# Kernel optimization log

Measured on AMD Instinct MI355X. Metric: run time of the kernel, lower is better.

## Reference

```python
import jax, jax.numpy as jnp
import numpy as np

D_MODEL = 1024
N_HEADS = 16
HEAD_DIM = D_MODEL // N_HEADS


def setup_inputs() -> dict:
    key = jax.random.key(0)
    ks = jax.random.split(key, 5)
    B, S = 4, 2048
    scale = 1.0 / np.sqrt(D_MODEL)
    return {
        "x": jax.random.normal(ks[0], (B, S, D_MODEL), dtype=jnp.float32),
        "W_q": jax.random.normal(ks[1], (D_MODEL, D_MODEL), dtype=jnp.float32) * scale,
        "W_k": jax.random.normal(ks[2], (D_MODEL, D_MODEL), dtype=jnp.float32) * scale,
        "W_v": jax.random.normal(ks[3], (D_MODEL, D_MODEL), dtype=jnp.float32) * scale,
        "W_o": jax.random.normal(ks[4], (D_MODEL, D_MODEL), dtype=jnp.float32) * scale,
    }


def reference(x, W_q, W_k, W_v, W_o):
    B, S, _ = x.shape
    # nn.Linear(d,d,bias=False): y = x @ W.T ; W stored as (out,in)
    def proj(W):
        y = jnp.einsum('bsd,ed->bse', x, W)
        return y.reshape(B, S, N_HEADS, HEAD_DIM).transpose(0, 2, 1, 3)  # (B,H,S,Dh)
    q, k, v = proj(W_q), proj(W_k), proj(W_v)
    scores = jnp.einsum('bhqd,bhkd->bhqk', q, k) / np.sqrt(HEAD_DIM)
    causal = jnp.tril(jnp.ones((S, S), dtype=bool))  # (S,S)
    scores = jnp.where(causal[None, None], scores, -jnp.inf)
    attn = jax.nn.softmax(scores, axis=-1)
    heads = jnp.einsum('bhqk,bhkd->bhqd', attn, v)
    concat = heads.transpose(0, 2, 1, 3).reshape(B, S, D_MODEL)
    return jnp.einsum('bsd,ed->bse', concat, W_o)
```

## Files before the change

### kernel.cpp

```cpp
#include <hip/hip_runtime.h>
#include <hip/hip_bf16.h>

#define D_MODEL 1024
#define N_HEADS 16
#define HEAD_DIM 64
#define BATCH 4
#define SEQ 2048
#define M_ROWS (BATCH * SEQ)

typedef __attribute__((ext_vector_type(8))) __bf16 bf16x8;
typedef __attribute__((ext_vector_type(8))) short short8;
typedef __attribute__((ext_vector_type(4))) float f32x4;

static __device__ __forceinline__ unsigned short f2bf_rne(float f) {
  unsigned int u = __float_as_uint(f);
  u += 0x7FFFu + ((u >> 16) & 1u);
  return (unsigned short)(u >> 16);
}

#if __has_builtin(__builtin_amdgcn_exp2f)
#define EXP2F(x) __builtin_amdgcn_exp2f(x)
#else
#define EXP2F(x) exp2f(x)
#endif

static __device__ __forceinline__ void gl_lds16(const unsigned short* g, unsigned short* l) {
  __builtin_amdgcn_global_load_lds((const __attribute__((address_space(1))) unsigned int*)g,
                                   (__attribute__((address_space(3))) unsigned int*)l, 16, 0, 0);
}

__global__ __launch_bounds__(256) void cvt_all(const float* __restrict__ x,
                                               const float* __restrict__ wq,
                                               const float* __restrict__ wk,
                                               const float* __restrict__ wv,
                                               const float* __restrict__ wo,
                                               unsigned short* __restrict__ xb,
                                               unsigned short* __restrict__ wqb,
                                               unsigned short* __restrict__ wkb,
                                               unsigned short* __restrict__ wvb,
                                               unsigned short* __restrict__ wob) {
  const int bid = blockIdx.x;
  const float* src;
  unsigned short* dst;
  int i;
  if (bid < 8192) {
    src = x; dst = xb; i = bid * 256 + threadIdx.x;
  } else {
    int r = bid - 8192;
    int w = r >> 10;
    i = (r & 1023) * 256 + threadIdx.x;
    switch (w) {
      case 0: src = wq; dst = wqb; break;
      case 1: src = wk; dst = wkb; break;
      case 2: src = wv; dst = wvb; break;
      default: src = wo; dst = wob; break;
    }
  }
  float4 f = reinterpret_cast<const float4*>(src)[i];
  ushort4 o;
  o.x = f2bf_rne(f.x); o.y = f2bf_rne(f.y); o.z = f2bf_rne(f.z); o.w = f2bf_rne(f.w);
  reinterpret_cast<ushort4*>(dst)[i] = o;
}

__global__ __launch_bounds__(256) void qkv_gemm(const unsigned short* __restrict__ A,
                                                const unsigned short* __restrict__ Wq,
                                                const unsigned short* __restrict__ Wk,
                                                const unsigned short* __restrict__ Wv,
                                                unsigned short* __restrict__ Qo,
                                                unsigned short* __restrict__ Ko,
                                                unsigned short* __restrict__ Vt) {
  __shared__ __align__(16) unsigned short smem[16384];
  const int t = threadIdx.x;
  const int widx = blockIdx.x >> 3;
  const int bn = blockIdx.x & 7, bm = blockIdx.y;
  const unsigned short* Bw = (widx == 0) ? Wq : (widx == 1) ? Wk : Wv;
  const float oscale = (widx == 0) ? 0.18033688f : 1.0f;
  const int K = D_MODEL, N = D_MODEL;

  const int wave = t >> 6, lane = t & 63;
  const int wm = (wave >> 1) * 64, wn = (wave & 1) * 64;
  const int lr = lane & 15, quad = lane >> 4;
  const int rxor = (lr >> 1) & 3;

  const int g0 = wave * 128 + lane, g1 = g0 + 64;
  const int r0 = g0 >> 2, c0 = (((g0 & 3) ^ ((r0 >> 1) & 3)) << 3);
  const int r1 = g1 >> 2, c1 = (((g1 & 3) ^ ((r1 >> 1) & 3)) << 3);
  const unsigned short* Arow0 = A + (size_t)(bm * 128 + r0) * K + c0;
  const unsigned short* Arow1 = A + (size_t)(bm * 128 + r1) * K + c1;
  const unsigned short* Brow0 = Bw + (size_t)(bn * 128 + r0) * K + c0;
  const unsigned short* Brow1 = Bw + (size_t)(bn * 128 + r1) * K + c1;

  f32x4 acc[4][4] = {};

  gl_lds16(Arow0, &smem[g0 * 8]);
  gl_lds16(Arow1, &smem[g1 * 8]);
  gl_lds16(Brow0, &smem[4096 + g0 * 8]);
  gl_lds16(Brow1, &smem[4096 + g1 * 8]);
  __syncthreads();

  for (int it = 0; it < 32; it++) {
    const int cur = (it & 1) * 8192;
    if (it + 1 < 32) {
      const int nxt = 8192 - cur;
      const int k1 = (it + 1) * 32;
      gl_lds16(Arow0 + k1, &smem[nxt + g0 * 8]);
      gl_lds16(Arow1 + k1, &smem[nxt + g1 * 8]);
      gl_lds16(Brow0 + k1, &smem[nxt + 4096 + g0 * 8]);
      gl_lds16(Brow1 + k1, &smem[nxt + 4096 + g1 * 8]);
    }
    const unsigned short* As = &smem[cur];
    const unsigned short* Bs = &smem[cur + 4096];

    bf16x8 af[4], bfr[4];
#pragma unroll
    for (int mt = 0; mt < 4; mt++)
      af[mt] = __builtin_bit_cast(
          bf16x8,
          *reinterpret_cast<const short8*>(&As[(wm + mt * 16 + lr) * 32 + (quad ^ rxor) * 8]));
#pragma unroll
    for (int nt = 0; nt < 4; nt++)
      bfr[nt] = __builtin_bit_cast(
          bf16x8,
          *reinterpret_cast<const short8*>(&Bs[(wn + nt * 16 + lr) * 32 + (quad ^ rxor) * 8]));
#pragma unroll
    for (int mt = 0; mt < 4; mt++)
#pragma unroll
      for (int nt = 0; nt < 4; nt++)
        acc[mt][nt] = __builtin_amdgcn_mfma_f32_16x16x32_bf16(af[mt], bfr[nt], acc[mt][nt], 0, 0, 0);
    __syncthreads();
  }

  if (widx < 2) {
    unsigned short* Cp = (widx == 0) ? Qo : Ko;
#pragma unroll
    for (int mt = 0; mt < 4; mt++) {
#pragma unroll
      for (int nt = 0; nt < 4; nt++) {
        int col = bn * 128 + wn + nt * 16 + lr;
#pragma unroll
        for (int r = 0; r < 4; r++) {
          int row = bm * 128 + wm + mt * 16 + quad * 4 + r;
          Cp[(size_t)row * N + col] = f2bf_rne(acc[mt][nt][r] * oscale);
        }
      }
    }
  } else {
    const int b = bm >> 4;
    const int s0 = (bm & 15) * 128;
#pragma unroll
    for (int half = 0; half < 2; half++) {
      __syncthreads();
      if ((wave & 1) == half) {
#pragma unroll
        for (int nt = 0; nt < 4; nt++) {
#pragma unroll
          for (int mt = 0; mt < 4; mt++) {
#pragma unroll
            for (int r = 0; r < 4; r++) {
              int cl = nt * 16 + lr;
              int rl = wm + mt * 16 + quad * 4 + r;
              smem[cl * 136 + rl] = f2bf_rne(acc[mt][nt][r]);
            }
          }
        }
      }
      __syncthreads();
      const int h2 = bn * 2 + half;
      const size_t rowbase = ((size_t)(b * N_HEADS + h2)) * HEAD_DIM;
#pragma unroll
      for (int i = 0; i < 4; i++) {
        int c = i * 256 + t;
        int d = c >> 4, s8 = (c & 15) * 8;
        uint4 v = *reinterpret_cast<const uint4*>(&smem[d * 136 + s8]);
        *reinterpret_cast<uint4*>(Vt + (rowbase + d) * SEQ + s0 + s8) = v;
      }
    }
  }
}

__global__ __launch_bounds__(256) void gemm_bt_f32(const unsigned short* __restrict__ A,
                                                   const unsigned short* __restrict__ Bw,
                                                   float* __restrict__ Cp,
                                                   int M, int N, int K) {
  __shared__ __align__(16) unsigned short smem[16384];
  const int t = threadIdx.x;
  const int bn = blockIdx.x, bm = blockIdx.y;
  const int wave = t >> 6, lane = t & 63;
  const int wm = (wave >> 1) * 64, wn = (wave & 1) * 64;
  const int lr = lane & 15, quad = lane >> 4;
  const int rxor = (lr >> 1) & 3;

  const int g0 = wave * 128 + lane, g1 = g0 + 64;
  const int r0 = g0 >> 2, c0 = (((g0 & 3) ^ ((r0 >> 1) & 3)) << 3);
  const int r1 = g1 >> 2, c1 = (((g1 & 3) ^ ((r1 >> 1) & 3)) << 3);
  const unsigned short* Arow0 = A + (size_t)(bm * 128 + r0) * K + c0;
  const unsigned short* Arow1 = A + (size_t)(bm * 128 + r1) * K + c1;
  const unsigned short* Brow0 = Bw + (size_t)(bn * 128 + r0) * K + c0;
  const unsigned short* Brow1 = Bw + (size_t)(bn * 128 + r1) * K + c1;

  f32x4 acc[4][4] = {};

  gl_lds16(Arow0, &smem[g0 * 8]);
  gl_lds16(Arow1, &smem[g1 * 8]);
  gl_lds16(Brow0, &smem[4096 + g0 * 8]);
  gl_lds16(Brow1, &smem[4096 + g1 * 8]);
  __syncthreads();

  for (int it = 0; it < 32; it++) {
    const int cur = (it & 1) * 8192;
    if (it + 1 < 32) {
      const int nxt = 8192 - cur;
      const int k1 = (it + 1) * 32;
      gl_lds16(Arow0 + k1, &smem[nxt + g0 * 8]);
      gl_lds16(Arow1 + k1, &smem[nxt + g1 * 8]);
      gl_lds16(Brow0 + k1, &smem[nxt + 4096 + g0 * 8]);
      gl_lds16(Brow1 + k1, &smem[nxt + 4096 + g1 * 8]);
    }
    const unsigned short* As = &smem[cur];
    const unsigned short* Bs = &smem[cur + 4096];

    bf16x8 af[4], bfr[4];
#pragma unroll
    for (int mt = 0; mt < 4; mt++)
      af[mt] = __builtin_bit_cast(
          bf16x8,
          *reinterpret_cast<const short8*>(&As[(wm + mt * 16 + lr) * 32 + (quad ^ rxor) * 8]));
#pragma unroll
    for (int nt = 0; nt < 4; nt++)
      bfr[nt] = __builtin_bit_cast(
          bf16x8,
          *reinterpret_cast<const short8*>(&Bs[(wn + nt * 16 + lr) * 32 + (quad ^ rxor) * 8]));
#pragma unroll
    for (int mt = 0; mt < 4; mt++)
#pragma unroll
      for (int nt = 0; nt < 4; nt++)
        acc[mt][nt] = __builtin_amdgcn_mfma_f32_16x16x32_bf16(af[mt], bfr[nt], acc[mt][nt], 0, 0, 0);
    __syncthreads();
  }

#pragma unroll
  for (int mt = 0; mt < 4; mt++) {
#pragma unroll
    for (int nt = 0; nt < 4; nt++) {
      int col = bn * 128 + wn + nt * 16 + lr;
#pragma unroll
      for (int r = 0; r < 4; r++) {
        int row = bm * 128 + wm + mt * 16 + quad * 4 + r;
        Cp[(size_t)row * N + col] = acc[mt][nt][r];
      }
    }
  }
}

__global__ __launch_bounds__(512, 4) void attn_causal(const unsigned short* __restrict__ Q,
                                                      const unsigned short* __restrict__ Km,
                                                      const unsigned short* __restrict__ Vt,
                                                      unsigned short* __restrict__ O) {
  __shared__ __align__(16) unsigned short Kv[2][2][64 * 64];
  __shared__ __align__(16) unsigned short Ps[8][16 * 72];

  const int bid = blockIdx.x;
  const int p = bid & 7;
  const int h = (bid >> 3) & 15;
  const int b = bid >> 7;

  const int t = threadIdx.x;
  const int wave = t >> 6, lane = t & 63;
  const int lr = lane & 15, quad = lane >> 4;
  const int cxor = lr & 7;

  const size_t base = (size_t)b * SEQ * D_MODEL + h * HEAD_DIM;
  const unsigned short* Qb = Q + base;
  const unsigned short* Kb = Km + base;
  const unsigned short* Vb = Vt + (size_t)(b * N_HEADS + h) * HEAD_DIM * SEQ;
  unsigned short* pw = &Ps[wave][0];

  const int srow = t >> 3;
  const int scol = ((t & 7) ^ (srow & 7)) << 3;
  const unsigned short* Kg = Kb + (size_t)srow * D_MODEL + scol;
  const unsigned short* Vg = Vb + (size_t)srow * SEQ + scol;

  for (int ph = 0; ph < 2; ph++) {
    const int qt = ph ? (15 - p) : p;
    const int m0 = qt * 128 + wave * 16;
    const int ntiles = (qt + 1) * 2;

    bf16x8 qf[2];
#pragma unroll
    for (int kk = 0; kk < 2; kk++)
      qf[kk] = __builtin_bit_cast(
          bf16x8,
          *reinterpret_cast<const short8*>(Qb + (size_t)(m0 + lr) * D_MODEL + kk * 32 + quad * 8));

    f32x4 o_acc[4] = {};
    float lsum[4] = {};

    gl_lds16(Kg, &Kv[0][0][t * 8]);
    gl_lds16(Vg, &Kv[0][1][t * 8]);

    for (int kt = 0; kt < ntiles; kt++) {
      const int cur = kt & 1;
      const int kv0 = kt * 64;
      __syncthreads();
      if (kt + 1 < ntiles) {
        gl_lds16(Kg + (size_t)(kv0 + 64) * D_MODEL, &Kv[1 - cur][0][t * 8]);
        gl_lds16(Vg + kv0 + 64, &Kv[1 - cur][1][t * 8]);
      }
      const unsigned short* Ks = &Kv[cur][0][0];
      const unsigned short* Vs = &Kv[cur][1][0];

      f32x4 sAcc[4] = {};
#pragma unroll
      for (int kk = 0; kk < 2; kk++) {
        bf16x8 kf[4];
#pragma unroll
        for (int j = 0; j < 4; j++)
          kf[j] = __builtin_bit_cast(
              bf16x8, *reinterpret_cast<const short8*>(
                          &Ks[(j * 16 + lr) * 64 + ((kk * 4 + quad) ^ cxor) * 8]));
#pragma unroll
        for (int j = 0; j < 4; j++)
          sAcc[j] = __builtin_amdgcn_mfma_f32_16x16x32_bf16(qf[kk], kf[j], sAcc[j], 0, 0, 0);
      }

      asm volatile("s_waitcnt lgkmcnt(0)" ::: "memory");
      const bool needmask = (kv0 + 63 > m0);
#pragma unroll
      for (int r = 0; r < 4; r++) {
        const int qpos = m0 + quad * 4 + r;
        float e[4];
#pragma unroll
        for (int j = 0; j < 4; j++) e[j] = EXP2F(sAcc[j][r]);
        if (needmask) {
#pragma unroll
          for (int j = 0; j < 4; j++)
            if (kv0 + j * 16 + lr > qpos) e[j] = 0.f;
        }
        lsum[r] += (e[0] + e[1]) + (e[2] + e[3]);
        unsigned short* pr = &pw[(quad * 4 + r) * 72];
#pragma unroll
        for (int j = 0; j < 4; j++) pr[j * 16 + lr] = f2bf_rne(e[j]);
      }
      asm volatile("s_waitcnt lgkmcnt(0)" ::: "memory");

#pragma unroll
      for (int kk = 0; kk < 2; kk++) {
        bf16x8 pf = __builtin_bit_cast(
            bf16x8, *reinterpret_cast<const short8*>(&pw[lr * 72 + kk * 32 + quad * 8]));
#pragma unroll
        for (int c = 0; c < 4; c++) {
          bf16x8 vv = __builtin_bit_cast(
              bf16x8, *reinterpret_cast<const short8*>(
                          &Vs[(c * 16 + lr) * 64 + ((kk * 4 + quad) ^ cxor) * 8]));
          o_acc[c] = __builtin_amdgcn_mfma_f32_16x16x32_bf16(pf, vv, o_acc[c], 0, 0, 0);
        }
      }
    }

#pragma unroll
    for (int r = 0; r < 4; r++) {
      float l = lsum[r];
#pragma unroll
      for (int off = 1; off < 16; off <<= 1) l += __shfl_xor(l, off, 64);
      const float inv = 1.f / l;
      const int qpos = m0 + quad * 4 + r;
#pragma unroll
      for (int c = 0; c < 4; c++)
        O[base + (size_t)qpos * D_MODEL + c * 16 + lr] = f2bf_rne(o_acc[c][r] * inv);
    }
  }
}

extern "C" void kernel_launch(void* const* d_in, const int* in_sizes, int n_in,
                              void* d_out, int out_size, void* d_ws, size_t ws_size,
                              hipStream_t stream) {
  const float* x  = (const float*)d_in[0];
  const float* Wq = (const float*)d_in[1];
  const float* Wk = (const float*)d_in[2];
  const float* Wv = (const float*)d_in[3];
  const float* Wo = (const float*)d_in[4];
  float* out = (float*)d_out;

  char* ws = (char*)d_ws;
  const size_t SZ_X = (size_t)M_ROWS * D_MODEL * 2;
  const size_t SZ_W = (size_t)D_MODEL * D_MODEL * 2;
  unsigned short* xb  = (unsigned short*)(ws);
  unsigned short* wqb = (unsigned short*)(ws + SZ_X);
  unsigned short* wkb = (unsigned short*)(ws + SZ_X + 1 * SZ_W);
  unsigned short* wvb = (unsigned short*)(ws + SZ_X + 2 * SZ_W);
  unsigned short* wob = (unsigned short*)(ws + SZ_X + 3 * SZ_W);
  unsigned short* Qb  = (unsigned short*)(ws + 1 * SZ_X + 4 * SZ_W);
  unsigned short* Kb  = (unsigned short*)(ws + 2 * SZ_X + 4 * SZ_W);
  unsigned short* Vt  = (unsigned short*)(ws + 3 * SZ_X + 4 * SZ_W);
  unsigned short* Ob  = xb;

  cvt_all<<<12288, 256, 0, stream>>>(x, Wq, Wk, Wv, Wo, xb, wqb, wkb, wvb, wob);

  qkv_gemm<<<dim3(24, 64), 256, 0, stream>>>(xb, wqb, wkb, wvb, Qb, Kb, Vt);

  attn_causal<<<512, 512, 0, stream>>>(Qb, Kb, Vt, Ob);

  gemm_bt_f32<<<dim3(8, 64), 256, 0, stream>>>(Ob, wob, out, M_ROWS, D_MODEL, D_MODEL);
}
```

Baseline: 259.3 us.

## Rewrite QKV GEMM as 256x256 8-wave pipelined kernel with setprio

Replaces the 128x128, 4-wave QKV projection GEMM with a 256x256-tile, 512-thread kernel. It uses a 64-wide K step, 128 KB of LDS staging and a hand-scheduled prefetch interleaved with the MFMA phases via explicit barriers and vmcnt waits, plus a remapped block order for L2 locality. The aim is more operand reuse per loaded byte and better overlap of global loads with compute. It also raises wave priority around MFMA blocks in the attention kernel. Risks are lower occupancy, high register pressure from 32 accumulators, and subtle synchronization errors in the custom pipeline.

Measured after the change: 245.9 us. -5.2%, faster.

```diff
diff --git a/kernel.cpp b/kernel.cpp
--- a/kernel.cpp
+++ b/kernel.cpp
@@ -28,6 +28,10 @@
   __builtin_amdgcn_global_load_lds((const __attribute__((address_space(1))) unsigned int*)g,
                                    (__attribute__((address_space(3))) unsigned int*)l, 16, 0, 0);
 }
+
+#define BAR() asm volatile("s_barrier" ::: "memory")
+#define WAIT_LGKM0() asm volatile("s_waitcnt lgkmcnt(0)" ::: "memory")
+#define WAIT_VM(N) asm volatile("s_waitcnt vmcnt(" #N ")" ::: "memory")
 
 __global__ __launch_bounds__(256) void cvt_all(const float* __restrict__ x,
                                                const float* __restrict__ wq,
@@ -62,117 +66,157 @@
   reinterpret_cast<ushort4*>(dst)[i] = o;
 }
 
-__global__ __launch_bounds__(256) void qkv_gemm(const unsigned short* __restrict__ A,
-                                                const unsigned short* __restrict__ Wq,
-                                                const unsigned short* __restrict__ Wk,
-                                                const unsigned short* __restrict__ Wv,
-                                                unsigned short* __restrict__ Qo,
-                                                unsigned short* __restrict__ Ko,
-                                                unsigned short* __restrict__ Vt) {
-  __shared__ __align__(16) unsigned short smem[16384];
+__global__ __launch_bounds__(512, 2) void qkv_gemm8(const unsigned short* __restrict__ A,
+                                                    const unsigned short* __restrict__ Wq,
+                                                    const unsigned short* __restrict__ Wk,
+                                                    const unsigned short* __restrict__ Wv,
+                                                    unsigned short* __restrict__ Qo,
+                                                    unsigned short* __restrict__ Ko,
+                                                    unsigned short* __restrict__ Vt) {
+  __shared__ __align__(16) unsigned short smem[65536];
+
+  const int bid = blockIdx.x;
+  const int wgid = (bid & 7) * 48 + (bid >> 3);
+  const int widx = wgid >> 7;
+  const int rem = wgid & 127;
+  const int bm = rem >> 2, bn = rem & 3;
+
+  const unsigned short* Bw = (widx == 0) ? Wq : (widx == 1) ? Wk : Wv;
+
   const int t = threadIdx.x;
-  const int widx = blockIdx.x >> 3;
-  const int bn = blockIdx.x & 7, bm = blockIdx.y;
-  const unsigned short* Bw = (widx == 0) ? Wq : (widx == 1) ? Wk : Wv;
-  const float oscale = (widx == 0) ? 0.18033688f : 1.0f;
-  const int K = D_MODEL, N = D_MODEL;
-
   const int wave = t >> 6, lane = t & 63;
-  const int wm = (wave >> 1) * 64, wn = (wave & 1) * 64;
+  const int wmi = wave >> 2, wni = wave & 3;
   const int lr = lane & 15, quad = lane >> 4;
-  const int rxor = (lr >> 1) & 3;
-
-  const int g0 = wave * 128 + lane, g1 = g0 + 64;
-  const int r0 = g0 >> 2, c0 = (((g0 & 3) ^ ((r0 >> 1) & 3)) << 3);
-  const int r1 = g1 >> 2, c1 = (((g1 & 3) ^ ((r1 >> 1) & 3)) << 3);
-  const unsigned short* Arow0 = A + (size_t)(bm * 128 + r0) * K + c0;
-  const unsigned short* Arow1 = A + (size_t)(bm * 128 + r1) * K + c1;
-  const unsigned short* Brow0 = Bw + (size_t)(bn * 128 + r0) * K + c0;
-  const unsigned short* Brow1 = Bw + (size_t)(bn * 128 + r1) * K + c1;
-
-  f32x4 acc[4][4] = {};
-
-  gl_lds16(Arow0, &smem[g0 * 8]);
-  gl_lds16(Arow1, &smem[g1 * 8]);
-  gl_lds16(Brow0, &smem[4096 + g0 * 8]);
-  gl_lds16(Brow1, &smem[4096 + g1 * 8]);
-  __syncthreads();
-
-  for (int it = 0; it < 32; it++) {
-    const int cur = (it & 1) * 8192;
-    if (it + 1 < 32) {
-      const int nxt = 8192 - cur;
-      const int k1 = (it + 1) * 32;
-      gl_lds16(Arow0 + k1, &smem[nxt + g0 * 8]);
-      gl_lds16(Arow1 + k1, &smem[nxt + g1 * 8]);
-      gl_lds16(Brow0 + k1, &smem[nxt + 4096 + g0 * 8]);
-      gl_lds16(Brow1 + k1, &smem[nxt + 4096 + g1 * 8]);
-    }
-    const unsigned short* As = &smem[cur];
-    const unsigned short* Bs = &smem[cur + 4096];
-
-    bf16x8 af[4], bfr[4];
-#pragma unroll
-    for (int mt = 0; mt < 4; mt++)
-      af[mt] = __builtin_bit_cast(
-          bf16x8,
-          *reinterpret_cast<const short8*>(&As[(wm + mt * 16 + lr) * 32 + (quad ^ rxor) * 8]));
-#pragma unroll
-    for (int nt = 0; nt < 4; nt++)
-      bfr[nt] = __builtin_bit_cast(
-          bf16x8,
-          *reinterpret_cast<const short8*>(&Bs[(wn + nt * 16 + lr) * 32 + (quad ^ rxor) * 8]));
-#pragma unroll
-    for (int mt = 0; mt < 4; mt++)
-#pragma unroll
-      for (int nt = 0; nt < 4; nt++)
-        acc[mt][nt] = __builtin_amdgcn_mfma_f32_16x16x32_bf16(af[mt], bfr[nt], acc[mt][nt], 0, 0, 0);
-    __syncthreads();
+
+  const int r0 = t >> 3, c0 = (t & 7) ^ (r0 & 7);
+  const int s1 = t + 512;
+  const int r1 = s1 >> 3, c1 = (s1 & 7) ^ (r1 & 7);
+  const unsigned short* Asrc0 = A + (size_t)(bm * 256 + r0) * D_MODEL + c0 * 8;
+  const unsigned short* Asrc1 = A + (size_t)(bm * 256 + r1) * D_MODEL + c1 * 8;
+  const unsigned short* Bsrc0 = Bw + (size_t)(bn * 256 + r0) * D_MODEL + c0 * 8;
+  const unsigned short* Bsrc1 = Bw + (size_t)(bn * 256 + r1) * D_MODEL + c1 * 8;
+
+  auto stageA = [&](int kt, int buf, int half) {
+    unsigned short* dst = &smem[(buf * 2 + half) * 8192];
+    const size_t go = (size_t)half * (128 * D_MODEL) + kt * 64;
+    gl_lds16(Asrc0 + go, dst + t * 8);
+    gl_lds16(Asrc1 + go, dst + s1 * 8);
+  };
+  auto stageB = [&](int kt, int buf, int half) {
+    unsigned short* dst = &smem[32768 + (buf * 2 + half) * 8192];
+    const size_t go = (size_t)half * (128 * D_MODEL) + kt * 64;
+    gl_lds16(Bsrc0 + go, dst + t * 8);
+    gl_lds16(Bsrc1 + go, dst + s1 * 8);
+  };
+
+  f32x4 acc[8][4] = {};
+  bf16x8 bfrag[4][2];
+
+  stageA(0, 0, 0); stageA(0, 0, 1);
+  stageB(0, 0, 0); stageB(0, 0, 1);
+  stageB(1, 1, 0); stageB(1, 1, 1);
+  WAIT_VM(4);
+  BAR();
+
+  const int brow0 = (wni & 1) * 64;
+  for (int j = 0; j < 8; ++j) {
+#pragma unroll
+    for (int tb = 0; tb < 2; ++tb) {
+      const unsigned short* As = &smem[(tb * 2 + wmi) * 8192];
+      const unsigned short* Bs = &smem[32768 + (tb * 2 + (wni >> 1)) * 8192];
+#pragma unroll
+      for (int qd = 0; qd < 4; ++qd) {
+        const int p = tb * 4 + qd;
+        if (qd == 0) {
+#pragma unroll
+          for (int n = 0; n < 4; ++n)
+#pragma unroll
+            for (int ks = 0; ks < 2; ++ks) {
+              const int row = brow0 + n * 16 + lr;
+              bfrag[n][ks] = __builtin_bit_cast(
+                  bf16x8, *reinterpret_cast<const short8*>(
+                              &Bs[row * 64 + (((ks * 4 + quad) ^ (row & 7)) * 8)]));
+            }
+        }
+        bf16x8 af[2][2];
+#pragma unroll
+        for (int mi = 0; mi < 2; ++mi)
+#pragma unroll
+          for (int ks = 0; ks < 2; ++ks) {
+            const int row = (qd * 2 + mi) * 16 + lr;
+            af[mi][ks] = __builtin_bit_cast(
+                bf16x8, *reinterpret_cast<const short8*>(
+                            &As[row * 64 + (((ks * 4 + quad) ^ (row & 7)) * 8)]));
+          }
+        if (p == 0) stageA(2 * j + 1, 1, 0);
+        if (p == 1) { stageA(2 * j + 1, 1, 1); if (j < 7) stageB(2 * j + 2, 0, 0); }
+        if (p == 2) { if (j < 7) stageB(2 * j + 2, 0, 1); }
+        if (p == 4) { if (j < 7) stageA(2 * j + 2, 0, 0); }
+        if (p == 5) { if (j < 7) { stageA(2 * j + 2, 0, 1); stageB(2 * j + 3, 1, 0); } }
+        if (p == 6) { if (j < 7) stageB(2 * j + 3, 1, 1); }
+        BAR();
+        WAIT_LGKM0();
+        __builtin_amdgcn_s_setprio(1);
+#pragma unroll
+        for (int mi = 0; mi < 2; ++mi)
+#pragma unroll
+          for (int n = 0; n < 4; ++n)
+#pragma unroll
+            for (int ks = 0; ks < 2; ++ks)
+              acc[qd * 2 + mi][n] = __builtin_amdgcn_mfma_f32_16x16x32_bf16(
+                  af[mi][ks], bfrag[n][ks], acc[qd * 2 + mi][n], 0, 0, 0);
+        __builtin_amdgcn_s_setprio(0);
+        if (p == 3) { if (j < 7) { WAIT_VM(4); } else { WAIT_VM(0); } }
+        if (p == 7) { if (j < 7) { WAIT_VM(4); } }
+        BAR();
+      }
+    }
   }
 
   if (widx < 2) {
     unsigned short* Cp = (widx == 0) ? Qo : Ko;
-#pragma unroll
-    for (int mt = 0; mt < 4; mt++) {
-#pragma unroll
-      for (int nt = 0; nt < 4; nt++) {
-        int col = bn * 128 + wn + nt * 16 + lr;
-#pragma unroll
-        for (int r = 0; r < 4; r++) {
-          int row = bm * 128 + wm + mt * 16 + quad * 4 + r;
-          Cp[(size_t)row * N + col] = f2bf_rne(acc[mt][nt][r] * oscale);
+    const float sc = (widx == 0) ? 0.18033688f : 1.0f;
+#pragma unroll
+    for (int m = 0; m < 8; ++m) {
+#pragma unroll
+      for (int n = 0; n < 4; ++n) {
+        const int col = bn * 256 + wni * 64 + n * 16 + lr;
+#pragma unroll
+        for (int r = 0; r < 4; ++r) {
+          const int row = bm * 256 + wmi * 128 + m * 16 + quad * 4 + r;
+          Cp[(size_t)row * D_MODEL + col] = f2bf_rne(acc[m][n][r] * sc);
         }
       }
     }
   } else {
-    const int b = bm >> 4;
-    const int s0 = (bm & 15) * 128;
-#pragma unroll
-    for (int half = 0; half < 2; half++) {
+    const int b = bm >> 3;
+    const int s0 = (bm & 7) * 256;
+#pragma unroll
+    for (int h = 0; h < 2; ++h) {
       __syncthreads();
-      if ((wave & 1) == half) {
-#pragma unroll
-        for (int nt = 0; nt < 4; nt++) {
-#pragma unroll
-          for (int mt = 0; mt < 4; mt++) {
-#pragma unroll
-            for (int r = 0; r < 4; r++) {
-              int cl = nt * 16 + lr;
-              int rl = wm + mt * 16 + quad * 4 + r;
-              smem[cl * 136 + rl] = f2bf_rne(acc[mt][nt][r]);
+      if (wmi == h) {
+#pragma unroll
+        for (int n = 0; n < 4; ++n) {
+          const int d = wni * 64 + n * 16 + lr;
+#pragma unroll
+          for (int m = 0; m < 8; ++m) {
+#pragma unroll
+            for (int r = 0; r < 4; ++r) {
+              const int srow = m * 16 + quad * 4 + r;
+              smem[d * 136 + srow] = f2bf_rne(acc[m][n][r]);
             }
           }
         }
       }
       __syncthreads();
-      const int h2 = bn * 2 + half;
-      const size_t rowbase = ((size_t)(b * N_HEADS + h2)) * HEAD_DIM;
-#pragma unroll
-      for (int i = 0; i < 4; i++) {
-        int c = i * 256 + t;
-        int d = c >> 4, s8 = (c & 15) * 8;
+#pragma unroll
+      for (int i = 0; i < 8; ++i) {
+        const int c = i * 512 + t;
+        const int d = c >> 4, s8 = (c & 15) * 8;
         uint4 v = *reinterpret_cast<const uint4*>(&smem[d * 136 + s8]);
-        *reinterpret_cast<uint4*>(Vt + (rowbase + d) * SEQ + s0 + s8) = v;
+        const int h2 = bn * 4 + (d >> 6);
+        const size_t rowbase = (size_t)(b * N_HEADS + h2) * HEAD_DIM + (d & 63);
+        *reinterpret_cast<uint4*>(Vt + rowbase * SEQ + s0 + h * 128 + s8) = v;
       }
     }
   }
@@ -310,6 +354,7 @@
       const unsigned short* Vs = &Kv[cur][1][0];
 
       f32x4 sAcc[4] = {};
+      __builtin_amdgcn_s_setprio(1);
 #pragma unroll
       for (int kk = 0; kk < 2; kk++) {
         bf16x8 kf[4];
@@ -322,6 +367,7 @@
         for (int j = 0; j < 4; j++)
           sAcc[j] = __builtin_amdgcn_mfma_f32_16x16x32_bf16(qf[kk], kf[j], sAcc[j], 0, 0, 0);
       }
+      __builtin_amdgcn_s_setprio(0);
 
       asm volatile("s_waitcnt lgkmcnt(0)" ::: "memory");
       const bool needmask = (kv0 + 63 > m0);
@@ -343,6 +389,7 @@
       }
       asm volatile("s_waitcnt lgkmcnt(0)" ::: "memory");
 
+      __builtin_amdgcn_s_setprio(1);
 #pragma unroll
       for (int kk = 0; kk < 2; kk++) {
         bf16x8 pf = __builtin_bit_cast(
@@ -355,6 +402,7 @@
           o_acc[c] = __builtin_amdgcn_mfma_f32_16x16x32_bf16(pf, vv, o_acc[c], 0, 0, 0);
         }
       }
+      __builtin_amdgcn_s_setprio(0);
     }
 
 #pragma unroll
@@ -396,7 +444,7 @@
 
   cvt_all<<<12288, 256, 0, stream>>>(x, Wq, Wk, Wv, Wo, xb, wqb, wkb, wvb, wob);
 
-  qkv_gemm<<<dim3(24, 64), 256, 0, stream>>>(xb, wqb, wkb, wvb, Qb, Kb, Vt);
+  qkv_gemm8<<<384, 512, 0, stream>>>(xb, wqb, wkb, wvb, Qb, Kb, Vt);
 
   attn_causal<<<512, 512, 0, stream>>>(Qb, Kb, Vt, Ob);
 
```
